# Optimization experiments

Hardware: AMD Instinct MI355X
Metric: run time of the kernel (lower is better)

Reference implementation:

```python
import jax, jax.numpy as jnp
import numpy as np

B, V, D = 128, 1024, 512

def setup_inputs() -> dict:
    key = jax.random.key(0)
    ks = jax.random.split(key, 6)
    return {
        "features": jax.random.normal(ks[0], (B, D), dtype=jnp.float32),
        "phoneme_counts": jax.random.uniform(ks[1], (V,), minval=0.01, maxval=1.0, dtype=jnp.float32),
        "total_count": jnp.asarray(float(V), dtype=jnp.float32),
        "meg_prototypes": jax.random.normal(ks[2], (V, D), dtype=jnp.float32),
        "zipf_s": jnp.asarray(1.0, dtype=jnp.float32),
        "temperature": jnp.asarray(1.0, dtype=jnp.float32),
        "W1": jax.random.normal(ks[3], (D, 2 * D), dtype=jnp.float32) * 0.02,
        "b1": jnp.zeros((D,), dtype=jnp.float32),
        "W2": jax.random.normal(ks[4], (1, D), dtype=jnp.float32) * 0.02,
        "b2": jnp.zeros((1,), dtype=jnp.float32),
    }

def _l2norm(x, axis=-1, eps=1e-12):
    n = jnp.sqrt(jnp.sum(x * x, axis=axis, keepdims=True))
    return x / jnp.maximum(n, eps)

def reference(features, phoneme_counts, total_count, meg_prototypes,
              zipf_s, temperature, W1, b1, W2, b2):
    vocab = phoneme_counts.shape[0]
    d = features.shape[1]
    # Zipf weights: rank phonemes by frequency (descending), weight = rank^{-s}
    freqs = phoneme_counts / jnp.maximum(total_count, 1.0)
    order = jnp.argsort(-freqs)  # indices sorted by descending frequency
    ranks = jnp.zeros_like(freqs).at[order].set(
        jnp.arange(1, vocab + 1, dtype=freqs.dtype))
    zw = jnp.power(jnp.maximum(ranks, 1.0), -zipf_s)
    zipf_priors = zw / jnp.maximum(zw.sum(), 1e-8)  # [V]
    # Cosine similarity / temperature
    sim = _l2norm(features) @ _l2norm(meg_prototypes).T  # [B, V]
    sim = sim / jnp.maximum(temperature, 1e-4)
    # MLP attention: split Linear(2D,D) into feature and prototype halves,
    # avoiding the materialized [B,V,2D] concat.
    Wf, Wp = W1[:, :d], W1[:, d:]  # each [D, D]
    feat_part = features @ Wf.T          # [B, D]
    proto_part = meg_prototypes @ Wp.T   # [V, D]
    h = jax.nn.relu(feat_part[:, None, :] + proto_part[None, :, :] + b1)  # [B, V, D]
    attn = jax.nn.sigmoid(jnp.einsum('bvd,d->bv', h, W2[0]) + b2[0])      # [B, V]
    weights = zipf_priors[None, :] * (1.0 + sim) * attn
    return jax.nn.softmax(weights, axis=-1)
```

## Files before the change

### kernel.cpp

```cpp
#include <hip/hip_runtime.h>
#include <hip/hip_bf16.h>


typedef __attribute__((ext_vector_type(8))) short bhalf8;
typedef __attribute__((ext_vector_type(4))) float f32x4;

static __device__ __forceinline__ unsigned short f2bf(float x) {
    union { __hip_bfloat16 h; unsigned short u; } cv;
    cv.h = __float2bfloat16(x);
    return cv.u;
}

static __device__ __forceinline__ int4 pack_bf16_8(float4 x, float4 y) {
    union { ushort u[8]; int4 v; } r;
    r.u[0] = f2bf(x.x); r.u[1] = f2bf(x.y); r.u[2] = f2bf(x.z); r.u[3] = f2bf(x.w);
    r.u[4] = f2bf(y.x); r.u[5] = f2bf(y.y); r.u[6] = f2bf(y.z); r.u[7] = f2bf(y.w);
    return r.v;
}

__global__ __launch_bounds__(256) void gemm_prep_kernel(
    const float* __restrict__ feat, const float* __restrict__ counts,
    const float* __restrict__ proto, const float* __restrict__ zs,
    const float* __restrict__ W1, const float* __restrict__ b1,
    float* __restrict__ fpT, unsigned short* __restrict__ ppbT,
    float* __restrict__ dotraw,
    float* __restrict__ zw, float* __restrict__ invf, float* __restrict__ invp)
{
    int bx = blockIdx.x, tid = threadIdx.x;

    if (bx >= 176) {
        if (bx < 192) {
            __shared__ float cn[1024];
            ((float4*)cn)[tid] = ((const float4*)counts)[tid];
            __syncthreads();
            int il = tid >> 2, q = tid & 3;
            int i = (bx - 176) * 64 + il;
            float ci = cn[i];
            int cnt = 0;
            int j0 = q * 256;
            for (int j = j0; j < j0 + 256; ++j) {
                float cj = cn[j];
                cnt += (cj > ci) ? 1 : 0;
                cnt += (cj == ci && j < i) ? 1 : 0;
            }
            cnt += __shfl_xor(cnt, 1);
            cnt += __shfl_xor(cnt, 2);
            if (q == 0) zw[i] = powf((float)(cnt + 1), -zs[0]);
        } else {
            int nb = bx - 192;
            int w = tid >> 6, lane = tid & 63;
            int row = nb * 4 + w;
            const float* src = (row < 128) ? (feat + (size_t)row * 512)
                                           : (proto + (size_t)(row - 128) * 512);
            const float4* rp = (const float4*)src;
            float4 a = rp[lane * 2], b = rp[lane * 2 + 1];
            float ss = a.x*a.x + a.y*a.y + a.z*a.z + a.w*a.w
                     + b.x*b.x + b.y*b.y + b.z*b.z + b.w*b.w;
            for (int o = 32; o; o >>= 1) ss += __shfl_xor(ss, o);
            if (lane == 0) {
                float inv = 1.0f / fmaxf(sqrtf(ss), 1e-12f);
                if (row < 128) invf[row] = inv; else invp[row - 128] = inv;
            }
        }
        return;
    }

    const float* A; const float* Bm;
    int lda, ldb, tm, tn, mode;
    if (bx < 16) {
        A = feat; lda = 512; Bm = W1; ldb = 1024; mode = 0;
        tm = bx >> 3; tn = bx & 7;
    } else if (bx < 144) {
        int t = bx - 16;
        A = W1 + 512; lda = 1024; Bm = proto; ldb = 512; mode = 1;
        tm = t >> 4; tn = t & 15;
    } else {
        int t = bx - 144;
        A = feat; lda = 512; Bm = proto; ldb = 512; mode = 2;
        tm = t >> 4; tn = t & 15;
    }

    __shared__ unsigned short As[2][64 * 72];
    __shared__ unsigned short Bs[2][64 * 72];

    int r = tid >> 2, kq = (tid & 3) * 16;
    int wave = tid >> 6, lane = tid & 63;
    int fr = lane & 15, quad = lane >> 4;

    const float* Ag = A + (size_t)(tm * 64 + r) * lda + kq;
    const float* Bg = Bm + (size_t)(tn * 64 + r) * ldb + kq;

    float4 a0 = *(const float4*)(Ag),      a1 = *(const float4*)(Ag + 4);
    float4 a2 = *(const float4*)(Ag + 8),  a3 = *(const float4*)(Ag + 12);
    float4 g0 = *(const float4*)(Bg),      g1 = *(const float4*)(Bg + 4);
    float4 g2 = *(const float4*)(Bg + 8),  g3 = *(const float4*)(Bg + 12);

    f32x4 acc0 = {0.f, 0.f, 0.f, 0.f};
    f32x4 acc1 = acc0, acc2 = acc0, acc3 = acc0;

    for (int kc = 0; kc < 512; kc += 64) {
        int p = (kc >> 6) & 1;
        *(int4*)&As[p][r * 72 + kq]     = pack_bf16_8(a0, a1);
        *(int4*)&As[p][r * 72 + kq + 8] = pack_bf16_8(a2, a3);
        *(int4*)&Bs[p][r * 72 + kq]     = pack_bf16_8(g0, g1);
        *(int4*)&Bs[p][r * 72 + kq + 8] = pack_bf16_8(g2, g3);
        __syncthreads();
        if (kc + 64 < 512) {
            const float* An = Ag + kc + 64;
            const float* Bn = Bg + kc + 64;
            a0 = *(const float4*)(An);     a1 = *(const float4*)(An + 4);
            a2 = *(const float4*)(An + 8); a3 = *(const float4*)(An + 12);
            g0 = *(const float4*)(Bn);     g1 = *(const float4*)(Bn + 4);
            g2 = *(const float4*)(Bn + 8); g3 = *(const float4*)(Bn + 12);
        }
        #pragma unroll
        for (int s = 0; s < 2; ++s) {
            int ko = s * 32 + quad * 8;
            bhalf8 af  = *(const bhalf8*)&As[p][(wave * 16 + fr) * 72 + ko];
            bhalf8 bf0 = *(const bhalf8*)&Bs[p][(fr) * 72 + ko];
            bhalf8 bf1 = *(const bhalf8*)&Bs[p][(16 + fr) * 72 + ko];
            bhalf8 bf2 = *(const bhalf8*)&Bs[p][(32 + fr) * 72 + ko];
            bhalf8 bf3 = *(const bhalf8*)&Bs[p][(48 + fr) * 72 + ko];
            acc0 = __builtin_amdgcn_mfma_f32_16x16x32_bf16(af, bf0, acc0, 0, 0, 0);
            acc1 = __builtin_amdgcn_mfma_f32_16x16x32_bf16(af, bf1, acc1, 0, 0, 0);
            acc2 = __builtin_amdgcn_mfma_f32_16x16x32_bf16(af, bf2, acc2, 0, 0, 0);
            acc3 = __builtin_amdgcn_mfma_f32_16x16x32_bf16(af, bf3, acc3, 0, 0, 0);
        }
    }

    int m0 = tm * 64 + wave * 16 + quad * 4;
    int n0 = tn * 64 + fr;
    f32x4 accs[4] = {acc0, acc1, acc2, acc3};
    if (mode == 0) {
        for (int j = 0; j < 4; ++j)
            for (int rr = 0; rr < 4; ++rr)
                fpT[(size_t)(n0 + j * 16) * 128 + m0 + rr] = accs[j][rr];
    } else if (mode == 1) {
        float bv4[4];
        for (int rr = 0; rr < 4; ++rr) bv4[rr] = b1[m0 + rr];
        for (int j = 0; j < 4; ++j)
            for (int rr = 0; rr < 4; ++rr)
                ppbT[(size_t)(m0 + rr) * 1024 + n0 + j * 16] = f2bf(accs[j][rr] + bv4[rr]);
    } else {
        for (int j = 0; j < 4; ++j)
            for (int rr = 0; rr < 4; ++rr)
                dotraw[(size_t)(m0 + rr) * 1024 + n0 + j * 16] = accs[j][rr];
    }
}

__global__ __launch_bounds__(256) void hs_kernel(
    const float* __restrict__ fpT, const unsigned short* __restrict__ ppbT,
    const float* __restrict__ W2, float* __restrict__ hsp)
{
    int bx = blockIdx.x, tid = threadIdx.x;
    int bg = bx & 31, vh = (bx >> 5) & 1, ks = bx >> 6;
    int b0 = bg * 4, v = vh * 512 + tid * 2, k0 = ks * 32;

    float acc[4][2] = {};
    #pragma unroll 8
    for (int kk = 0; kk < 32; ++kk) {
        int k = k0 + kk;
        unsigned int u = *(const unsigned int*)(ppbT + (size_t)k * 1024 + v);
        float px = __uint_as_float(u << 16);
        float py = __uint_as_float(u & 0xffff0000u);
        float w2k = W2[k];
        float4 fa = *(const float4*)(fpT + (size_t)k * 128 + b0);
        float f[4] = {fa.x, fa.y, fa.z, fa.w};
        #pragma unroll
        for (int i = 0; i < 4; ++i) {
            acc[i][0] += fmaxf(f[i] + px, 0.f) * w2k;
            acc[i][1] += fmaxf(f[i] + py, 0.f) * w2k;
        }
    }
    float* o = hsp + ((size_t)ks * 128 + b0) * 1024 + v;
    #pragma unroll
    for (int i = 0; i < 4; ++i)
        *(float2*)(o + (size_t)i * 1024) = make_float2(acc[i][0], acc[i][1]);
}

__global__ __launch_bounds__(1024) void combine_kernel(
    const float* __restrict__ dotraw, const float* __restrict__ hsp,
    const float* __restrict__ zw,
    const float* __restrict__ invf, const float* __restrict__ invp,
    const float* __restrict__ temp, const float* __restrict__ b2,
    float* __restrict__ out)
{
    int b = blockIdx.x, tid = threadIdx.x;
    int wave = tid >> 6, lane = tid & 63;
    int v = tid;
    __shared__ float red[16];

    float it  = invf[b] / fmaxf(temp[0], 1e-4f);
    float b2v = b2[0];

    float zwv = zw[v];
    float dr  = dotraw[(size_t)b * 1024 + v];
    float ipv = invp[v];

    float h = 0.f;
    #pragma unroll
    for (int s = 0; s < 16; ++s)
        h += hsp[((size_t)s * 128 + b) * 1024 + v];

    float zs4 = zwv;
    for (int o = 32; o; o >>= 1) zs4 += __shfl_xor(zs4, o);
    if (lane == 0) red[wave] = zs4;
    __syncthreads();
    float zsum = 0.f;
    #pragma unroll
    for (int i = 0; i < 16; ++i) zsum += red[i];
    float izw = 1.0f / fmaxf(zsum, 1e-8f);
    __syncthreads();

    float sim = dr * it * ipv;
    float g = h + b2v;
    float w = (zwv * izw) * (1.0f + sim) * (1.0f / (1.0f + expf(-g)));

    float mx = w;
    for (int o = 32; o; o >>= 1) mx = fmaxf(mx, __shfl_xor(mx, o));
    if (lane == 0) red[wave] = mx;
    __syncthreads();
    mx = red[0];
    #pragma unroll
    for (int i = 1; i < 16; ++i) mx = fmaxf(mx, red[i]);
    __syncthreads();

    float e = expf(w - mx);
    float sm = e;
    for (int o = 32; o; o >>= 1) sm += __shfl_xor(sm, o);
    if (lane == 0) red[wave] = sm;
    __syncthreads();
    float tot = 0.f;
    #pragma unroll
    for (int i = 0; i < 16; ++i) tot += red[i];

    out[(size_t)b * 1024 + v] = e / tot;
}

extern "C" void kernel_launch(void* const* d_in, const int* in_sizes, int n_in,
                              void* d_out, int out_size, void* d_ws, size_t ws_size,
                              hipStream_t stream) {
    const float* feat   = (const float*)d_in[0];
    const float* counts = (const float*)d_in[1];
    const float* proto  = (const float*)d_in[3];
    const float* zs     = (const float*)d_in[4];
    const float* temp   = (const float*)d_in[5];
    const float* W1     = (const float*)d_in[6];
    const float* b1     = (const float*)d_in[7];
    const float* W2     = (const float*)d_in[8];
    const float* b2     = (const float*)d_in[9];

    char* ws = (char*)d_ws;
    float* zw     = (float*)(ws + 0);
    float* invf   = (float*)(ws + 4096);
    float* invp   = (float*)(ws + 4608);
    float* fpT    = (float*)(ws + 8704);
    float* dotraw = (float*)(ws + 270848);
    unsigned short* ppbT = (unsigned short*)(ws + 795136);
    float* hsp    = (float*)(ws + 1843712);

    gemm_prep_kernel<<<480, 256, 0, stream>>>(feat, counts, proto, zs, W1, b1,
                                              fpT, ppbT, dotraw, zw, invf, invp);
    hs_kernel<<<1024, 256, 0, stream>>>(fpT, ppbT, W2, hsp);
    combine_kernel<<<128, 1024, 0, stream>>>(dotraw, hsp, zw, invf, invp,
                                             temp, b2, (float*)d_out);
}
```

Before: 100.4 us.

## Fuse GEMM prep, hidden-sum and softmax into one cooperative kernel

Replaces the three separate launches with a single cooperative kernel that uses grid-wide syncs between phases: the GEMM/prep phase, a hidden-sum phase and a softmax phase. The hidden-sum phase no longer splits K across blocks into partial sums. Instead, 256 blocks each loop over all 512 k for 2 batch rows and 256 vocab entries, and write final weights directly. This is meant to remove launch gaps and the partial-sum buffer round trip. In exchange, the heavy phase runs with far fewer threads and longer serial loops, and two grid syncs are added.

```diff
diff --git a/kernel.cpp b/kernel.cpp
--- a/kernel.cpp
+++ b/kernel.cpp
@@ -1,5 +1,8 @@
 #include <hip/hip_runtime.h>
 #include <hip/hip_bf16.h>
+#include <hip/hip_cooperative_groups.h>
+
+namespace cg = cooperative_groups;
 
 
 typedef __attribute__((ext_vector_type(8))) short bhalf8;
@@ -9,6 +12,10 @@
     union { __hip_bfloat16 h; unsigned short u; } cv;
     cv.h = __float2bfloat16(x);
     return cv.u;
+}
+
+static __device__ __forceinline__ float bf2f(unsigned short u) {
+    return __uint_as_float(((unsigned int)u) << 16);
 }
 
 static __device__ __forceinline__ int4 pack_bf16_8(float4 x, float4 y) {
@@ -18,223 +25,206 @@
     return r.v;
 }
 
-__global__ __launch_bounds__(256) void gemm_prep_kernel(
+__global__ __launch_bounds__(256, 2) void fused_kernel(
     const float* __restrict__ feat, const float* __restrict__ counts,
     const float* __restrict__ proto, const float* __restrict__ zs,
-    const float* __restrict__ W1, const float* __restrict__ b1,
+    const float* __restrict__ temp, const float* __restrict__ W1,
+    const float* __restrict__ b1, const float* __restrict__ W2,
+    const float* __restrict__ b2,
     float* __restrict__ fpT, unsigned short* __restrict__ ppbT,
-    float* __restrict__ dotraw,
-    float* __restrict__ zw, float* __restrict__ invf, float* __restrict__ invp)
+    float* __restrict__ dotraw, float* __restrict__ zw,
+    float* __restrict__ invf, float* __restrict__ invp,
+    float* __restrict__ wbuf, float* __restrict__ out)
 {
+    cg::grid_group grid = cg::this_grid();
     int bx = blockIdx.x, tid = threadIdx.x;
-
-    if (bx >= 176) {
-        if (bx < 192) {
-            __shared__ float cn[1024];
-            ((float4*)cn)[tid] = ((const float4*)counts)[tid];
-            __syncthreads();
-            int il = tid >> 2, q = tid & 3;
-            int i = (bx - 176) * 64 + il;
-            float ci = cn[i];
-            int cnt = 0;
-            int j0 = q * 256;
-            for (int j = j0; j < j0 + 256; ++j) {
-                float cj = cn[j];
-                cnt += (cj > ci) ? 1 : 0;
-                cnt += (cj == ci && j < i) ? 1 : 0;
-            }
-            cnt += __shfl_xor(cnt, 1);
-            cnt += __shfl_xor(cnt, 2);
-            if (q == 0) zw[i] = powf((float)(cnt + 1), -zs[0]);
-        } else {
-            int nb = bx - 192;
-            int w = tid >> 6, lane = tid & 63;
-            int row = nb * 4 + w;
-            const float* src = (row < 128) ? (feat + (size_t)row * 512)
-                                           : (proto + (size_t)(row - 128) * 512);
-            const float4* rp = (const float4*)src;
-            float4 a = rp[lane * 2], b = rp[lane * 2 + 1];
-            float ss = a.x*a.x + a.y*a.y + a.z*a.z + a.w*a.w
-                     + b.x*b.x + b.y*b.y + b.z*b.z + b.w*b.w;
-            for (int o = 32; o; o >>= 1) ss += __shfl_xor(ss, o);
-            if (lane == 0) {
-                float inv = 1.0f / fmaxf(sqrtf(ss), 1e-12f);
-                if (row < 128) invf[row] = inv; else invp[row - 128] = inv;
-            }
-        }
-        return;
-    }
-
-    const float* A; const float* Bm;
-    int lda, ldb, tm, tn, mode;
-    if (bx < 16) {
-        A = feat; lda = 512; Bm = W1; ldb = 1024; mode = 0;
-        tm = bx >> 3; tn = bx & 7;
-    } else if (bx < 144) {
-        int t = bx - 16;
-        A = W1 + 512; lda = 1024; Bm = proto; ldb = 512; mode = 1;
-        tm = t >> 4; tn = t & 15;
-    } else {
-        int t = bx - 144;
-        A = feat; lda = 512; Bm = proto; ldb = 512; mode = 2;
-        tm = t >> 4; tn = t & 15;
-    }
 
     __shared__ unsigned short As[2][64 * 72];
     __shared__ unsigned short Bs[2][64 * 72];
-
-    int r = tid >> 2, kq = (tid & 3) * 16;
-    int wave = tid >> 6, lane = tid & 63;
-    int fr = lane & 15, quad = lane >> 4;
-
-    const float* Ag = A + (size_t)(tm * 64 + r) * lda + kq;
-    const float* Bg = Bm + (size_t)(tn * 64 + r) * ldb + kq;
-
-    float4 a0 = *(const float4*)(Ag),      a1 = *(const float4*)(Ag + 4);
-    float4 a2 = *(const float4*)(Ag + 8),  a3 = *(const float4*)(Ag + 12);
-    float4 g0 = *(const float4*)(Bg),      g1 = *(const float4*)(Bg + 4);
-    float4 g2 = *(const float4*)(Bg + 8),  g3 = *(const float4*)(Bg + 12);
-
-    f32x4 acc0 = {0.f, 0.f, 0.f, 0.f};
-    f32x4 acc1 = acc0, acc2 = acc0, acc3 = acc0;
-
-    for (int kc = 0; kc < 512; kc += 64) {
-        int p = (kc >> 6) & 1;
-        *(int4*)&As[p][r * 72 + kq]     = pack_bf16_8(a0, a1);
-        *(int4*)&As[p][r * 72 + kq + 8] = pack_bf16_8(a2, a3);
-        *(int4*)&Bs[p][r * 72 + kq]     = pack_bf16_8(g0, g1);
-        *(int4*)&Bs[p][r * 72 + kq + 8] = pack_bf16_8(g2, g3);
-        __syncthreads();
-        if (kc + 64 < 512) {
-            const float* An = Ag + kc + 64;
-            const float* Bn = Bg + kc + 64;
-            a0 = *(const float4*)(An);     a1 = *(const float4*)(An + 4);
-            a2 = *(const float4*)(An + 8); a3 = *(const float4*)(An + 12);
-            g0 = *(const float4*)(Bn);     g1 = *(const float4*)(Bn + 4);
-            g2 = *(const float4*)(Bn + 8); g3 = *(const float4*)(Bn + 12);
-        }
-        #pragma unroll
-        for (int s = 0; s < 2; ++s) {
-            int ko = s * 32 + quad * 8;
-            bhalf8 af  = *(const bhalf8*)&As[p][(wave * 16 + fr) * 72 + ko];
-            bhalf8 bf0 = *(const bhalf8*)&Bs[p][(fr) * 72 + ko];
-            bhalf8 bf1 = *(const bhalf8*)&Bs[p][(16 + fr) * 72 + ko];
-            bhalf8 bf2 = *(const bhalf8*)&Bs[p][(32 + fr) * 72 + ko];
-            bhalf8 bf3 = *(const bhalf8*)&Bs[p][(48 + fr) * 72 + ko];
-            acc0 = __builtin_amdgcn_mfma_f32_16x16x32_bf16(af, bf0, acc0, 0, 0, 0);
-            acc1 = __builtin_amdgcn_mfma_f32_16x16x32_bf16(af, bf1, acc1, 0, 0, 0);
-            acc2 = __builtin_amdgcn_mfma_f32_16x16x32_bf16(af, bf2, acc2, 0, 0, 0);
-            acc3 = __builtin_amdgcn_mfma_f32_16x16x32_bf16(af, bf3, acc3, 0, 0, 0);
+    __shared__ float red[16];
+
+    if (bx < 176) {
+        const float* A; const float* Bm;
+        int lda, ldb, tm, tn, mode;
+        if (bx < 16) {
+            A = feat; lda = 512; Bm = W1; ldb = 1024; mode = 0;
+            tm = bx >> 3; tn = bx & 7;
+        } else if (bx < 144) {
+            int t = bx - 16;
+            A = W1 + 512; lda = 1024; Bm = proto; ldb = 512; mode = 1;
+            tm = t >> 4; tn = t & 15;
+        } else {
+            int t = bx - 144;
+            A = feat; lda = 512; Bm = proto; ldb = 512; mode = 2;
+            tm = t >> 4; tn = t & 15;
+        }
+
+        int r = tid >> 2, kq = (tid & 3) * 16;
+        int wave = tid >> 6, lane = tid & 63;
+        int fr = lane & 15, quad = lane >> 4;
+
+        const float* Ag = A + (size_t)(tm * 64 + r) * lda + kq;
+        const float* Bg = Bm + (size_t)(tn * 64 + r) * ldb + kq;
+
+        float4 a0 = *(const float4*)(Ag),      a1 = *(const float4*)(Ag + 4);
+        float4 a2 = *(const float4*)(Ag + 8),  a3 = *(const float4*)(Ag + 12);
+        float4 g0 = *(const float4*)(Bg),      g1 = *(const float4*)(Bg + 4);
+        float4 g2 = *(const float4*)(Bg + 8),  g3 = *(const float4*)(Bg + 12);
+
+        f32x4 acc0 = {0.f, 0.f, 0.f, 0.f};
+        f32x4 acc1 = acc0, acc2 = acc0, acc3 = acc0;
+
+        for (int kc = 0; kc < 512; kc += 64) {
+            int p = (kc >> 6) & 1;
+            *(int4*)&As[p][r * 72 + kq]     = pack_bf16_8(a0, a1);
+            *(int4*)&As[p][r * 72 + kq + 8] = pack_bf16_8(a2, a3);
+            *(int4*)&Bs[p][r * 72 + kq]     = pack_bf16_8(g0, g1);
+            *(int4*)&Bs[p][r * 72 + kq + 8] = pack_bf16_8(g2, g3);
+            __syncthreads();
+            if (kc + 64 < 512) {
+                const float* An = Ag + kc + 64;
+                const float* Bn = Bg + kc + 64;
+                a0 = *(const float4*)(An);     a1 = *(const float4*)(An + 4);
+                a2 = *(const float4*)(An + 8); a3 = *(const float4*)(An + 12);
+                g0 = *(const float4*)(Bn);     g1 = *(const float4*)(Bn + 4);
+                g2 = *(const float4*)(Bn + 8); g3 = *(const float4*)(Bn + 12);
+            }
+            #pragma unroll
+            for (int s = 0; s < 2; ++s) {
+                int ko = s * 32 + quad * 8;
+                bhalf8 af  = *(const bhalf8*)&As[p][(wave * 16 + fr) * 72 + ko];
+                bhalf8 bf0 = *(const bhalf8*)&Bs[p][(fr) * 72 + ko];
+                bhalf8 bf1 = *(const bhalf8*)&Bs[p][(16 + fr) * 72 + ko];
+                bhalf8 bf2 = *(const bhalf8*)&Bs[p][(32 + fr) * 72 + ko];
+                bhalf8 bf3 = *(const bhalf8*)&Bs[p][(48 + fr) * 72 + ko];
+                acc0 = __builtin_amdgcn_mfma_f32_16x16x32_bf16(af, bf0, acc0, 0, 0, 0);
+                acc1 = __builtin_amdgcn_mfma_f32_16x16x32_bf16(af, bf1, acc1, 0, 0, 0);
+                acc2 = __builtin_amdgcn_mfma_f32_16x16x32_bf16(af, bf2, acc2, 0, 0, 0);
+                acc3 = __builtin_amdgcn_mfma_f32_16x16x32_bf16(af, bf3, acc3, 0, 0, 0);
+            }
+        }
+
+        int m0 = tm * 64 + wave * 16 + quad * 4;
+        int n0 = tn * 64 + fr;
+        f32x4 accs[4] = {acc0, acc1, acc2, acc3};
+        if (mode == 0) {
+            for (int j = 0; j < 4; ++j)
+                for (int rr = 0; rr < 4; ++rr)
+                    fpT[(size_t)(n0 + j * 16) * 128 + m0 + rr] = accs[j][rr];
+        } else if (mode == 1) {
+            float bv4[4];
+            for (int rr = 0; rr < 4; ++rr) bv4[rr] = b1[m0 + rr];
+            for (int j = 0; j < 4; ++j)
+                for (int rr = 0; rr < 4; ++rr)
+                    ppbT[(size_t)(m0 + rr) * 1024 + n0 + j * 16] = f2bf(accs[j][rr] + bv4[rr]);
+        } else {
+            for (int j = 0; j < 4; ++j)
+                for (int rr = 0; rr < 4; ++rr)
+                    dotraw[(size_t)(m0 + rr) * 1024 + n0 + j * 16] = accs[j][rr];
+        }
+    } else if (bx < 192) {
+        float* cn = (float*)&As[0][0];
+        ((float4*)cn)[tid] = ((const float4*)counts)[tid];
+        __syncthreads();
+        int il = tid >> 2, q = tid & 3;
+        int i = (bx - 176) * 64 + il;
+        float ci = cn[i];
+        int cnt = 0;
+        int j0 = q * 256;
+        for (int j = j0; j < j0 + 256; ++j) {
+            float cj = cn[j];
+            cnt += (cj > ci) ? 1 : 0;
+            cnt += (cj == ci && j < i) ? 1 : 0;
+        }
+        cnt += __shfl_xor(cnt, 1);
+        cnt += __shfl_xor(cnt, 2);
+        if (q == 0) zw[i] = powf((float)(cnt + 1), -zs[0]);
+    } else if (bx < 480) {
+        int nb = bx - 192;
+        int w = tid >> 6, lane = tid & 63;
+        int row = nb * 4 + w;
+        const float* src = (row < 128) ? (feat + (size_t)row * 512)
+                                       : (proto + (size_t)(row - 128) * 512);
+        const float4* rp = (const float4*)src;
+        float4 a = rp[lane * 2], b = rp[lane * 2 + 1];
+        float ss = a.x*a.x + a.y*a.y + a.z*a.z + a.w*a.w
+                 + b.x*b.x + b.y*b.y + b.z*b.z + b.w*b.w;
+        for (int o = 32; o; o >>= 1) ss += __shfl_xor(ss, o);
+        if (lane == 0) {
+            float inv = 1.0f / fmaxf(sqrtf(ss), 1e-12f);
+            if (row < 128) invf[row] = inv; else invp[row - 128] = inv;
         }
     }
 
-    int m0 = tm * 64 + wave * 16 + quad * 4;
-    int n0 = tn * 64 + fr;
-    f32x4 accs[4] = {acc0, acc1, acc2, acc3};
-    if (mode == 0) {
-        for (int j = 0; j < 4; ++j)
-            for (int rr = 0; rr < 4; ++rr)
-                fpT[(size_t)(n0 + j * 16) * 128 + m0 + rr] = accs[j][rr];
-    } else if (mode == 1) {
-        float bv4[4];
-        for (int rr = 0; rr < 4; ++rr) bv4[rr] = b1[m0 + rr];
-        for (int j = 0; j < 4; ++j)
-            for (int rr = 0; rr < 4; ++rr)
-                ppbT[(size_t)(m0 + rr) * 1024 + n0 + j * 16] = f2bf(accs[j][rr] + bv4[rr]);
-    } else {
-        for (int j = 0; j < 4; ++j)
-            for (int rr = 0; rr < 4; ++rr)
-                dotraw[(size_t)(m0 + rr) * 1024 + n0 + j * 16] = accs[j][rr];
+    grid.sync();
+
+    if (bx < 256) {
+        int wave = tid >> 6, lane = tid & 63;
+        int bg = bx >> 2, vq = bx & 3;
+        int b0 = bg * 2;
+        int v = vq * 256 + tid;
+
+        float4 z4 = ((const float4*)zw)[tid];
+        float zsl = z4.x + z4.y + z4.z + z4.w;
+        for (int o = 32; o; o >>= 1) zsl += __shfl_xor(zsl, o);
+        if (lane == 0) red[wave] = zsl;
+        __syncthreads();
+        float izw = 1.0f / fmaxf(red[0] + red[1] + red[2] + red[3], 1e-8f);
+
+        float itemp = 1.0f / fmaxf(temp[0], 1e-4f);
+        float it0 = invf[b0] * itemp, it1 = invf[b0 + 1] * itemp;
+        float b2v = b2[0];
+        float zwv = zw[v];
+        float ipv = invp[v];
+        float dr0 = dotraw[(size_t)b0 * 1024 + v];
+        float dr1 = dotraw[(size_t)(b0 + 1) * 1024 + v];
+
+        const unsigned short* pc = ppbT + v;
+        const float* fpb = fpT + b0;
+
+        float h0 = 0.f, h1 = 0.f;
+        #pragma unroll 8
+        for (int k = 0; k < 512; ++k) {
+            float p = bf2f(pc[(size_t)k << 10]);
+            float2 f = *(const float2*)(fpb + (size_t)k * 128);
+            float w2k = W2[k];
+            h0 += fmaxf(f.x + p, 0.f) * w2k;
+            h1 += fmaxf(f.y + p, 0.f) * w2k;
+        }
+
+        float w0 = (zwv * izw) * (1.0f + dr0 * it0 * ipv) * (1.0f / (1.0f + expf(-(h0 + b2v))));
+        float w1 = (zwv * izw) * (1.0f + dr1 * it1 * ipv) * (1.0f / (1.0f + expf(-(h1 + b2v))));
+        wbuf[(size_t)b0 * 1024 + v] = w0;
+        wbuf[(size_t)(b0 + 1) * 1024 + v] = w1;
     }
-}
-
-__global__ __launch_bounds__(256) void hs_kernel(
-    const float* __restrict__ fpT, const unsigned short* __restrict__ ppbT,
-    const float* __restrict__ W2, float* __restrict__ hsp)
-{
-    int bx = blockIdx.x, tid = threadIdx.x;
-    int bg = bx & 31, vh = (bx >> 5) & 1, ks = bx >> 6;
-    int b0 = bg * 4, v = vh * 512 + tid * 2, k0 = ks * 32;
-
-    float acc[4][2] = {};
-    #pragma unroll 8
-    for (int kk = 0; kk < 32; ++kk) {
-        int k = k0 + kk;
-        unsigned int u = *(const unsigned int*)(ppbT + (size_t)k * 1024 + v);
-        float px = __uint_as_float(u << 16);
-        float py = __uint_as_float(u & 0xffff0000u);
-        float w2k = W2[k];
-        float4 fa = *(const float4*)(fpT + (size_t)k * 128 + b0);
-        float f[4] = {fa.x, fa.y, fa.z, fa.w};
-        #pragma unroll
-        for (int i = 0; i < 4; ++i) {
-            acc[i][0] += fmaxf(f[i] + px, 0.f) * w2k;
-            acc[i][1] += fmaxf(f[i] + py, 0.f) * w2k;
-        }
+
+    grid.sync();
+
+    if (bx < 128) {
+        int wave = tid >> 6, lane = tid & 63;
+        int b = bx;
+        float4 w4 = *(const float4*)(wbuf + (size_t)b * 1024 + tid * 4);
+
+        float mx = fmaxf(fmaxf(w4.x, w4.y), fmaxf(w4.z, w4.w));
+        for (int o = 32; o; o >>= 1) mx = fmaxf(mx, __shfl_xor(mx, o));
+        if (lane == 0) red[wave] = mx;
+        __syncthreads();
+        mx = fmaxf(fmaxf(red[0], red[1]), fmaxf(red[2], red[3]));
+        __syncthreads();
+
+        float4 e;
+        e.x = expf(w4.x - mx); e.y = expf(w4.y - mx);
+        e.z = expf(w4.z - mx); e.w = expf(w4.w - mx);
+        float sm = e.x + e.y + e.z + e.w;
+        for (int o = 32; o; o >>= 1) sm += __shfl_xor(sm, o);
+        if (lane == 0) red[wave] = sm;
+        __syncthreads();
+        float inv = 1.0f / (red[0] + red[1] + red[2] + red[3]);
+
+        float4 r4;
+        r4.x = e.x * inv; r4.y = e.y * inv; r4.z = e.z * inv; r4.w = e.w * inv;
+        *(float4*)(out + (size_t)b * 1024 + tid * 4) = r4;
     }
-    float* o = hsp + ((size_t)ks * 128 + b0) * 1024 + v;
-    #pragma unroll
-    for (int i = 0; i < 4; ++i)
-        *(float2*)(o + (size_t)i * 1024) = make_float2(acc[i][0], acc[i][1]);
-}
-
-__global__ __launch_bounds__(1024) void combine_kernel(
-    const float* __restrict__ dotraw, const float* __restrict__ hsp,
-    const float* __restrict__ zw,
-    const float* __restrict__ invf, const float* __restrict__ invp,
-    const float* __restrict__ temp, const float* __restrict__ b2,
-    float* __restrict__ out)
-{
-    int b = blockIdx.x, tid = threadIdx.x;
-    int wave = tid >> 6, lane = tid & 63;
-    int v = tid;
-    __shared__ float red[16];
-
-    float it  = invf[b] / fmaxf(temp[0], 1e-4f);
-    float b2v = b2[0];
-
-    float zwv = zw[v];
-    float dr  = dotraw[(size_t)b * 1024 + v];
-    float ipv = invp[v];
-
-    float h = 0.f;
-    #pragma unroll
-    for (int s = 0; s < 16; ++s)
-        h += hsp[((size_t)s * 128 + b) * 1024 + v];
-
-    float zs4 = zwv;
-    for (int o = 32; o; o >>= 1) zs4 += __shfl_xor(zs4, o);
-    if (lane == 0) red[wave] = zs4;
-    __syncthreads();
-    float zsum = 0.f;
-    #pragma unroll
-    for (int i = 0; i < 16; ++i) zsum += red[i];
-    float izw = 1.0f / fmaxf(zsum, 1e-8f);
-    __syncthreads();
-
-    float sim = dr * it * ipv;
-    float g = h + b2v;
-    float w = (zwv * izw) * (1.0f + sim) * (1.0f / (1.0f + expf(-g)));
-
-    float mx = w;
-    for (int o = 32; o; o >>= 1) mx = fmaxf(mx, __shfl_xor(mx, o));
-    if (lane == 0) red[wave] = mx;
-    __syncthreads();
-    mx = red[0];
-    #pragma unroll
-    for (int i = 1; i < 16; ++i) mx = fmaxf(mx, red[i]);
-    __syncthreads();
-
-    float e = expf(w - mx);
-    float sm = e;
-    for (int o = 32; o; o >>= 1) sm += __shfl_xor(sm, o);
-    if (lane == 0) red[wave] = sm;
-    __syncthreads();
-    float tot = 0.f;
-    #pragma unroll
-    for (int i = 0; i < 16; ++i) tot += red[i];
-
-    out[(size_t)b * 1024 + v] = e / tot;
 }
 
 extern "C" void kernel_launch(void* const* d_in, const int* in_sizes, int n_in,
@@ -257,11 +247,15 @@
     float* fpT    = (float*)(ws + 8704);
     float* dotraw = (float*)(ws + 270848);
     unsigned short* ppbT = (unsigned short*)(ws + 795136);
-    float* hsp    = (float*)(ws + 1843712);
-
-    gemm_prep_kernel<<<480, 256, 0, stream>>>(feat, counts, proto, zs, W1, b1,
-                                              fpT, ppbT, dotraw, zw, invf, invp);
-    hs_kernel<<<1024, 256, 0, stream>>>(fpT, ppbT, W2, hsp);
-    combine_kernel<<<128, 1024, 0, stream>>>(dotraw, hsp, zw, invf, invp,
-                                             temp, b2, (float*)d_out);
-}
+    float* wbuf   = (float*)(ws + 1843712);
+    float* outp   = (float*)d_out;
+
+    void* args[] = {
+        (void*)&feat, (void*)&counts, (void*)&proto, (void*)&zs, (void*)&temp,
+        (void*)&W1, (void*)&b1, (void*)&W2, (void*)&b2,
+        (void*)&fpT, (void*)&ppbT, (void*)&dotraw, (void*)&zw,
+        (void*)&invf, (void*)&invp, (void*)&wbuf, (void*)&outp,
+    };
+    hipLaunchCooperativeKernel((void*)fused_kernel, dim3(512), dim3(256),
+                               args, 0, stream);
+}
```

Measured after the change: 237.3 us. 2.36x slower.

## Fuse hidden-sum into softmax head kernel and restage GEMM in two K halves

Applied to the files above, without the earlier changes.

Removes the separate hs_kernel and its 16-way split-K partial buffer. Each thread of the combined head kernel now loops over all 512 hidden units to compute its relu-MLP score before the softmax, eliminating one launch and the hsp round trip through memory. The GEMM prep kernel switches from a 64-wide double-buffered K loop to two 256-wide K stages with larger shared tiles and register-staged prefetch. The price is serial work per thread in the head kernel, which runs only 128 blocks and so exposes much less parallelism, plus higher register and LDS pressure in the GEMM.

```diff
diff --git a/kernel.cpp b/kernel.cpp
--- a/kernel.cpp
+++ b/kernel.cpp
@@ -9,6 +9,10 @@
     union { __hip_bfloat16 h; unsigned short u; } cv;
     cv.h = __float2bfloat16(x);
     return cv.u;
+}
+
+static __device__ __forceinline__ float bf2f(unsigned short u) {
+    return __uint_as_float(((unsigned int)u) << 16);
 }
 
 static __device__ __forceinline__ int4 pack_bf16_8(float4 x, float4 y) {
@@ -28,9 +32,12 @@
 {
     int bx = blockIdx.x, tid = threadIdx.x;
 
+    __shared__ unsigned short As[64 * 264];
+    __shared__ unsigned short Bs[64 * 264];
+
     if (bx >= 176) {
         if (bx < 192) {
-            __shared__ float cn[1024];
+            float* cn = (float*)&As[0];
             ((float4*)cn)[tid] = ((const float4*)counts)[tid];
             __syncthreads();
             int il = tid >> 2, q = tid & 3;
@@ -80,52 +87,71 @@
         tm = t >> 4; tn = t & 15;
     }
 
-    __shared__ unsigned short As[2][64 * 72];
-    __shared__ unsigned short Bs[2][64 * 72];
-
-    int r = tid >> 2, kq = (tid & 3) * 16;
+    int r = tid >> 2, q = tid & 3;
     int wave = tid >> 6, lane = tid & 63;
     int fr = lane & 15, quad = lane >> 4;
 
-    const float* Ag = A + (size_t)(tm * 64 + r) * lda + kq;
-    const float* Bg = Bm + (size_t)(tn * 64 + r) * ldb + kq;
-
-    float4 a0 = *(const float4*)(Ag),      a1 = *(const float4*)(Ag + 4);
-    float4 a2 = *(const float4*)(Ag + 8),  a3 = *(const float4*)(Ag + 12);
-    float4 g0 = *(const float4*)(Bg),      g1 = *(const float4*)(Bg + 4);
-    float4 g2 = *(const float4*)(Bg + 8),  g3 = *(const float4*)(Bg + 12);
+    const float* Ag = A + (size_t)(tm * 64 + r) * lda + q * 64;
+    const float* Bg = Bm + (size_t)(tn * 64 + r) * ldb + q * 64;
+    int lbase = r * 264 + q * 64;
 
     f32x4 acc0 = {0.f, 0.f, 0.f, 0.f};
     f32x4 acc1 = acc0, acc2 = acc0, acc3 = acc0;
 
-    for (int kc = 0; kc < 512; kc += 64) {
-        int p = (kc >> 6) & 1;
-        *(int4*)&As[p][r * 72 + kq]     = pack_bf16_8(a0, a1);
-        *(int4*)&As[p][r * 72 + kq + 8] = pack_bf16_8(a2, a3);
-        *(int4*)&Bs[p][r * 72 + kq]     = pack_bf16_8(g0, g1);
-        *(int4*)&Bs[p][r * 72 + kq + 8] = pack_bf16_8(g2, g3);
-        __syncthreads();
-        if (kc + 64 < 512) {
-            const float* An = Ag + kc + 64;
-            const float* Bn = Bg + kc + 64;
-            a0 = *(const float4*)(An);     a1 = *(const float4*)(An + 4);
-            a2 = *(const float4*)(An + 8); a3 = *(const float4*)(An + 12);
-            g0 = *(const float4*)(Bn);     g1 = *(const float4*)(Bn + 4);
-            g2 = *(const float4*)(Bn + 8); g3 = *(const float4*)(Bn + 12);
-        }
-        #pragma unroll
-        for (int s = 0; s < 2; ++s) {
-            int ko = s * 32 + quad * 8;
-            bhalf8 af  = *(const bhalf8*)&As[p][(wave * 16 + fr) * 72 + ko];
-            bhalf8 bf0 = *(const bhalf8*)&Bs[p][(fr) * 72 + ko];
-            bhalf8 bf1 = *(const bhalf8*)&Bs[p][(16 + fr) * 72 + ko];
-            bhalf8 bf2 = *(const bhalf8*)&Bs[p][(32 + fr) * 72 + ko];
-            bhalf8 bf3 = *(const bhalf8*)&Bs[p][(48 + fr) * 72 + ko];
-            acc0 = __builtin_amdgcn_mfma_f32_16x16x32_bf16(af, bf0, acc0, 0, 0, 0);
-            acc1 = __builtin_amdgcn_mfma_f32_16x16x32_bf16(af, bf1, acc1, 0, 0, 0);
-            acc2 = __builtin_amdgcn_mfma_f32_16x16x32_bf16(af, bf2, acc2, 0, 0, 0);
-            acc3 = __builtin_amdgcn_mfma_f32_16x16x32_bf16(af, bf3, acc3, 0, 0, 0);
-        }
+    float4 La[16], Lb[16];
+
+    #pragma unroll
+    for (int i = 0; i < 16; ++i) {
+        La[i] = *(const float4*)(Ag + i * 4);
+        Lb[i] = *(const float4*)(Bg + i * 4);
+    }
+    #pragma unroll
+    for (int j = 0; j < 8; ++j) {
+        *(int4*)&As[lbase + j * 8] = pack_bf16_8(La[2*j], La[2*j+1]);
+        *(int4*)&Bs[lbase + j * 8] = pack_bf16_8(Lb[2*j], Lb[2*j+1]);
+    }
+    __syncthreads();
+
+    #pragma unroll
+    for (int i = 0; i < 16; ++i) {
+        La[i] = *(const float4*)(Ag + 256 + i * 4);
+        Lb[i] = *(const float4*)(Bg + 256 + i * 4);
+    }
+
+    #pragma unroll
+    for (int s = 0; s < 8; ++s) {
+        int ko = s * 32 + quad * 8;
+        bhalf8 af  = *(const bhalf8*)&As[(wave * 16 + fr) * 264 + ko];
+        bhalf8 bf0 = *(const bhalf8*)&Bs[(fr) * 264 + ko];
+        bhalf8 bf1 = *(const bhalf8*)&Bs[(16 + fr) * 264 + ko];
+        bhalf8 bf2 = *(const bhalf8*)&Bs[(32 + fr) * 264 + ko];
+        bhalf8 bf3 = *(const bhalf8*)&Bs[(48 + fr) * 264 + ko];
+        acc0 = __builtin_amdgcn_mfma_f32_16x16x32_bf16(af, bf0, acc0, 0, 0, 0);
+        acc1 = __builtin_amdgcn_mfma_f32_16x16x32_bf16(af, bf1, acc1, 0, 0, 0);
+        acc2 = __builtin_amdgcn_mfma_f32_16x16x32_bf16(af, bf2, acc2, 0, 0, 0);
+        acc3 = __builtin_amdgcn_mfma_f32_16x16x32_bf16(af, bf3, acc3, 0, 0, 0);
+    }
+    __syncthreads();
+
+    #pragma unroll
+    for (int j = 0; j < 8; ++j) {
+        *(int4*)&As[lbase + j * 8] = pack_bf16_8(La[2*j], La[2*j+1]);
+        *(int4*)&Bs[lbase + j * 8] = pack_bf16_8(Lb[2*j], Lb[2*j+1]);
+    }
+    __syncthreads();
+
+    #pragma unroll
+    for (int s = 0; s < 8; ++s) {
+        int ko = s * 32 + quad * 8;
+        bhalf8 af  = *(const bhalf8*)&As[(wave * 16 + fr) * 264 + ko];
+        bhalf8 bf0 = *(const bhalf8*)&Bs[(fr) * 264 + ko];
+        bhalf8 bf1 = *(const bhalf8*)&Bs[(16 + fr) * 264 + ko];
+        bhalf8 bf2 = *(const bhalf8*)&Bs[(32 + fr) * 264 + ko];
+        bhalf8 bf3 = *(const bhalf8*)&Bs[(48 + fr) * 264 + ko];
+        acc0 = __builtin_amdgcn_mfma_f32_16x16x32_bf16(af, bf0, acc0, 0, 0, 0);
+        acc1 = __builtin_amdgcn_mfma_f32_16x16x32_bf16(af, bf1, acc1, 0, 0, 0);
+        acc2 = __builtin_amdgcn_mfma_f32_16x16x32_bf16(af, bf2, acc2, 0, 0, 0);
+        acc3 = __builtin_amdgcn_mfma_f32_16x16x32_bf16(af, bf3, acc3, 0, 0, 0);
     }
 
     int m0 = tm * 64 + wave * 16 + quad * 4;
@@ -148,63 +174,22 @@
     }
 }
 
-__global__ __launch_bounds__(256) void hs_kernel(
+__global__ __launch_bounds__(1024) void head_kernel(
     const float* __restrict__ fpT, const unsigned short* __restrict__ ppbT,
-    const float* __restrict__ W2, float* __restrict__ hsp)
-{
-    int bx = blockIdx.x, tid = threadIdx.x;
-    int bg = bx & 31, vh = (bx >> 5) & 1, ks = bx >> 6;
-    int b0 = bg * 4, v = vh * 512 + tid * 2, k0 = ks * 32;
-
-    float acc[4][2] = {};
-    #pragma unroll 8
-    for (int kk = 0; kk < 32; ++kk) {
-        int k = k0 + kk;
-        unsigned int u = *(const unsigned int*)(ppbT + (size_t)k * 1024 + v);
-        float px = __uint_as_float(u << 16);
-        float py = __uint_as_float(u & 0xffff0000u);
-        float w2k = W2[k];
-        float4 fa = *(const float4*)(fpT + (size_t)k * 128 + b0);
-        float f[4] = {fa.x, fa.y, fa.z, fa.w};
-        #pragma unroll
-        for (int i = 0; i < 4; ++i) {
-            acc[i][0] += fmaxf(f[i] + px, 0.f) * w2k;
-            acc[i][1] += fmaxf(f[i] + py, 0.f) * w2k;
-        }
-    }
-    float* o = hsp + ((size_t)ks * 128 + b0) * 1024 + v;
-    #pragma unroll
-    for (int i = 0; i < 4; ++i)
-        *(float2*)(o + (size_t)i * 1024) = make_float2(acc[i][0], acc[i][1]);
-}
-
-__global__ __launch_bounds__(1024) void combine_kernel(
-    const float* __restrict__ dotraw, const float* __restrict__ hsp,
-    const float* __restrict__ zw,
+    const float* __restrict__ dotraw, const float* __restrict__ zw,
     const float* __restrict__ invf, const float* __restrict__ invp,
-    const float* __restrict__ temp, const float* __restrict__ b2,
-    float* __restrict__ out)
+    const float* __restrict__ temp, const float* __restrict__ W2,
+    const float* __restrict__ b2, float* __restrict__ out)
 {
     int b = blockIdx.x, tid = threadIdx.x;
     int wave = tid >> 6, lane = tid & 63;
     int v = tid;
     __shared__ float red[16];
 
-    float it  = invf[b] / fmaxf(temp[0], 1e-4f);
-    float b2v = b2[0];
-
     float zwv = zw[v];
-    float dr  = dotraw[(size_t)b * 1024 + v];
-    float ipv = invp[v];
-
-    float h = 0.f;
-    #pragma unroll
-    for (int s = 0; s < 16; ++s)
-        h += hsp[((size_t)s * 128 + b) * 1024 + v];
-
-    float zs4 = zwv;
-    for (int o = 32; o; o >>= 1) zs4 += __shfl_xor(zs4, o);
-    if (lane == 0) red[wave] = zs4;
+    float zsl = zwv;
+    for (int o = 32; o; o >>= 1) zsl += __shfl_xor(zsl, o);
+    if (lane == 0) red[wave] = zsl;
     __syncthreads();
     float zsum = 0.f;
     #pragma unroll
@@ -212,9 +197,19 @@
     float izw = 1.0f / fmaxf(zsum, 1e-8f);
     __syncthreads();
 
-    float sim = dr * it * ipv;
-    float g = h + b2v;
-    float w = (zwv * izw) * (1.0f + sim) * (1.0f / (1.0f + expf(-g)));
+    const unsigned short* pc = ppbT + v;
+    float h = 0.f;
+    #pragma unroll 8
+    for (int k = 0; k < 512; ++k) {
+        float p = bf2f(pc[(size_t)k << 10]);
+        float f = fpT[(size_t)k * 128 + b];
+        float w2k = W2[k];
+        h += fmaxf(f + p, 0.f) * w2k;
+    }
+
+    float it  = invf[b] / fmaxf(temp[0], 1e-4f);
+    float sim = dotraw[(size_t)b * 1024 + v] * it * invp[v];
+    float w = (zwv * izw) * (1.0f + sim) * (1.0f / (1.0f + expf(-(h + b2[0]))));
 
     float mx = w;
     for (int o = 32; o; o >>= 1) mx = fmaxf(mx, __shfl_xor(mx, o));
@@ -257,11 +252,9 @@
     float* fpT    = (float*)(ws + 8704);
     float* dotraw = (float*)(ws + 270848);
     unsigned short* ppbT = (unsigned short*)(ws + 795136);
-    float* hsp    = (float*)(ws + 1843712);
 
     gemm_prep_kernel<<<480, 256, 0, stream>>>(feat, counts, proto, zs, W1, b1,
                                               fpT, ppbT, dotraw, zw, invf, invp);
-    hs_kernel<<<1024, 256, 0, stream>>>(fpT, ppbT, W2, hsp);
-    combine_kernel<<<128, 1024, 0, stream>>>(dotraw, hsp, zw, invf, invp,
-                                             temp, b2, (float*)d_out);
-}
+    head_kernel<<<128, 1024, 0, stream>>>(fpT, ppbT, dotraw, zw, invf, invp,
+                                          temp, W2, b2, (float*)d_out);
+}
```

Result: slower. 137.0 us (+36.4%).
